# Kernel tuning notes

Hardware: AMD Instinct MI355X
Metric: run time of the kernel (lower is better)

The kernel has to match this reference:

```python
import jax, jax.numpy as jnp
import numpy as np

B = 32768
NMU = 3
K = 8
TMAX = 31.41592653589793
DE = 128
NC = 64
ZC = 1
IN_DIM = K + K * NMU  # 32

FREQS = jnp.asarray(1.0 / (np.float32(TMAX) ** np.arange(K // 2, dtype=np.float32)))


def _sinenc(x):
    # x: (B,) or (B,d) -> (B, K) or (B, d*K); per-feature [sin|cos] blocks concatenated
    if x.ndim == 1:
        xw = x[:, None] * FREQS[None, :]
        return jnp.concatenate([jnp.sin(xw), jnp.cos(xw)], axis=1)
    xw = x[:, :, None] * FREQS[None, None, :]  # (B, d, K/2)
    return jnp.concatenate([jnp.sin(xw), jnp.cos(xw)], axis=2).reshape(x.shape[0], -1)


def _conv3(x, w, b):
    y = jax.lax.conv_general_dilated(x, w, window_strides=(1, 1), padding=((1, 1), (1, 1)),
                                     dimension_numbers=("NCHW", "OIHW", "NCHW"))
    return y + b[None, :, None, None]


def setup_inputs() -> dict:
    key = jax.random.key(0)
    ks = jax.random.split(key, 20)
    s = 0.05
    return {
        "t": jax.random.uniform(ks[0], (B,), jnp.float32) * TMAX,
        "z": jax.random.normal(ks[1], (B, ZC, 4, 4), jnp.float32),
        "mu": jax.random.normal(ks[2], (B, NMU), jnp.float32),
        "W1": jax.random.normal(ks[3], (IN_DIM, DE), jnp.float32) * s,
        "b1": jnp.zeros((DE,), jnp.float32),
        "W2": jax.random.normal(ks[4], (DE, DE), jnp.float32) * s,
        "b2": jnp.zeros((DE,), jnp.float32),
        "Wg": jax.random.normal(ks[5], (DE, 4 * NC), jnp.float32) * s,
        "bg": jnp.zeros((4 * NC,), jnp.float32),
        "cin_w": jax.random.normal(ks[6], (NC, ZC, 3, 3), jnp.float32) * s,
        "cin_b": jnp.zeros((NC,), jnp.float32),
        "c1_w": jax.random.normal(ks[7], (NC, NC, 3, 3), jnp.float32) * s,
        "c1_b": jnp.zeros((NC,), jnp.float32),
        "c2_w": jax.random.normal(ks[8], (NC, NC, 3, 3), jnp.float32) * s,
        "c2_b": jnp.zeros((NC,), jnp.float32),
        "cout_w": jax.random.normal(ks[9], (ZC, NC, 3, 3), jnp.float32) * s,
        "cout_b": jnp.zeros((ZC,), jnp.float32),
    }


def reference(t, z, mu, W1, b1, W2, b2, Wg, bg,
              cin_w, cin_b, c1_w, c1_b, c2_w, c2_b, cout_w, cout_b):
    t_emb = _sinenc(t)            # (B, K)
    mu_emb = _sinenc(mu)          # (B, K*nmu)
    x = jnp.concatenate([t_emb, mu_emb], axis=1)  # (B, in_dim)
    h = jax.nn.elu(x @ W1 + b1)
    xi = jax.nn.elu(h @ W2 + b2)
    gb = (xi @ Wg + bg).reshape(-1, 4, NC)
    g1 = gb[:, 0][:, :, None, None]
    g2 = gb[:, 1][:, :, None, None]
    bb1 = gb[:, 2][:, :, None, None]
    bb2 = gb[:, 3][:, :, None, None]
    hh = jnp.tanh(_conv3(z, cin_w, cin_b))
    hh = jnp.tanh(g1 * _conv3(hh, c1_w, c1_b) + bb1)
    hh = jnp.tanh(g2 * _conv3(hh, c2_w, c2_b) + bb2)
    return _conv3(hh, cout_w, cout_b)
```

## Files before the change

kernel.cpp:

```cpp
#include <hip/hip_runtime.h>
#include <cstdint>
#include <cstddef>


#define NB 32768

typedef _Float16 half8   __attribute__((ext_vector_type(8)));
typedef _Float16 half4_t __attribute__((ext_vector_type(4)));
typedef _Float16 half2_t __attribute__((ext_vector_type(2)));
typedef float    f32x4   __attribute__((ext_vector_type(4)));

__device__ __forceinline__ float fast_tanh(float x) {
  float e = __expf(2.0f * x);
  return 1.0f - __fdividef(2.0f, e + 1.0f);
}

__device__ __forceinline__ float elu_f(float v) {
  return v > 0.0f ? v : (__expf(v) - 1.0f);
}

__device__ __forceinline__ void conv_acc(float acc[16], const float r[16], const float w[9]) {
#pragma unroll
  for (int y = 0; y < 4; ++y)
#pragma unroll
    for (int x = 0; x < 4; ++x)
#pragma unroll
      for (int ky = 0; ky < 3; ++ky) {
        int iy = y + ky - 1;
        if (iy < 0 || iy >= 4) continue;
#pragma unroll
        for (int kx = 0; kx < 3; ++kx) {
          int ix = x + kx - 1;
          if (ix < 0 || ix >= 4) continue;
          acc[y * 4 + x] += w[ky * 3 + kx] * r[iy * 4 + ix];
        }
      }
}

__global__ __launch_bounds__(256) void prep_kernel(
    const float* __restrict__ W1, const float* __restrict__ W2,
    const float* __restrict__ Wg, const float* __restrict__ c1w,
    const float* __restrict__ c2w, _Float16* __restrict__ wt) {
  int idx = blockIdx.x * 256 + threadIdx.x;
  _Float16* W1t = wt;
  _Float16* W2t = W1t + 4096;
  _Float16* Wgt = W2t + 16384;
  _Float16* c1t = Wgt + 32768;
  _Float16* c2t = c1t + 36864;
  if (idx < 4096) {
    int n = idx >> 5, k = idx & 31;
    W1t[idx] = (_Float16)W1[k * 128 + n];
  } else if (idx < 20480) {
    int i = idx - 4096;
    int n = i >> 7, k = i & 127;
    W2t[i] = (_Float16)W2[k * 128 + n];
  } else if (idx < 53248) {
    int i = idx - 20480;
    int n = i >> 7, k = i & 127;
    Wgt[i] = (_Float16)Wg[k * 256 + n];
  } else if (idx < 90112) {
    int i = idx - 53248;
    int ts = i >> 11, r = i & 2047, oc = r >> 5, icw = r & 31;
    int tap = ts >> 1, kb = ts & 1, ic = kb * 32 + icw;
    c1t[i] = (_Float16)c1w[(oc * 64 + ic) * 9 + tap];
  } else if (idx < 126976) {
    int i = idx - 90112;
    int ts = i >> 11, r = i & 2047, oc = r >> 5, icw = r & 31;
    int tap = ts >> 1, kb = ts & 1, ic = kb * 32 + icw;
    c2t[i] = (_Float16)c2w[(oc * 64 + ic) * 9 + tap];
  }
}

__global__ __launch_bounds__(256) void mlp_kernel(
    const float* __restrict__ tt, const float* __restrict__ mu,
    const _Float16* __restrict__ wt,
    const float* __restrict__ b1, const float* __restrict__ b2,
    const float* __restrict__ bg, _Float16* __restrict__ gbf) {
  const int tid = threadIdx.x;
  const int lane = tid & 63;
  const int wv = tid >> 6;
  const int m = lane & 15, q = lane >> 4;
  const int q4 = q * 4, q8 = q * 8;
  const int s = blockIdx.x * 64 + wv * 16 + m;

  const _Float16* W1t = wt;
  const _Float16* W2t = W1t + 4096;
  const _Float16* Wgt = W2t + 16384;

  __shared__ __align__(16) _Float16 xi_lds[4][16 * 136];
  _Float16* xw = &xi_lds[wv][0];

  const float TM = 31.41592653589793f;
  float base = (q == 0) ? tt[s] : mu[(size_t)s * 3 + (q - 1)];
  half8 xb;
  float fr = 1.0f;
#pragma unroll
  for (int j = 0; j < 4; ++j) {
    float sn, cs;
    __sincosf(base * fr, &sn, &cs);
    xb[j] = (_Float16)sn;
    xb[4 + j] = (_Float16)cs;
    fr *= (1.0f / TM);
  }

#pragma unroll
  for (int nt = 0; nt < 8; ++nt) {
    half8 af = *(const half8*)(W1t + (nt * 16 + m) * 32 + q8);
    f32x4 c = __builtin_amdgcn_mfma_f32_16x16x32_f16(af, xb, (f32x4)(0.0f), 0, 0, 0);
    f32x4 bv = *(const f32x4*)(b1 + nt * 16 + q4);
    half4_t o;
#pragma unroll
    for (int r = 0; r < 4; ++r) o[r] = (_Float16)elu_f(c[r] + bv[r]);
    *(half4_t*)(xw + m * 136 + nt * 16 + q4) = o;
  }
  half8 xf0 = *(const half8*)(xw + m * 136 + 0 + q8);
  half8 xf1 = *(const half8*)(xw + m * 136 + 32 + q8);
  half8 xf2 = *(const half8*)(xw + m * 136 + 64 + q8);
  half8 xf3 = *(const half8*)(xw + m * 136 + 96 + q8);

#pragma unroll
  for (int nt = 0; nt < 8; ++nt) {
    const _Float16* wp = W2t + (nt * 16 + m) * 128;
    f32x4 c = (f32x4)(0.0f);
    c = __builtin_amdgcn_mfma_f32_16x16x32_f16(*(const half8*)(wp + q8), xf0, c, 0, 0, 0);
    c = __builtin_amdgcn_mfma_f32_16x16x32_f16(*(const half8*)(wp + 32 + q8), xf1, c, 0, 0, 0);
    c = __builtin_amdgcn_mfma_f32_16x16x32_f16(*(const half8*)(wp + 64 + q8), xf2, c, 0, 0, 0);
    c = __builtin_amdgcn_mfma_f32_16x16x32_f16(*(const half8*)(wp + 96 + q8), xf3, c, 0, 0, 0);
    f32x4 bv = *(const f32x4*)(b2 + nt * 16 + q4);
    half4_t o;
#pragma unroll
    for (int r = 0; r < 4; ++r) o[r] = (_Float16)elu_f(c[r] + bv[r]);
    *(half4_t*)(xw + m * 136 + nt * 16 + q4) = o;
  }
  half8 yf0 = *(const half8*)(xw + m * 136 + 0 + q8);
  half8 yf1 = *(const half8*)(xw + m * 136 + 32 + q8);
  half8 yf2 = *(const half8*)(xw + m * 136 + 64 + q8);
  half8 yf3 = *(const half8*)(xw + m * 136 + 96 + q8);

#pragma unroll
  for (int ut = 0; ut < 16; ++ut) {
    const _Float16* wp = Wgt + (ut * 16 + m) * 128;
    f32x4 c = (f32x4)(0.0f);
    c = __builtin_amdgcn_mfma_f32_16x16x32_f16(*(const half8*)(wp + q8), yf0, c, 0, 0, 0);
    c = __builtin_amdgcn_mfma_f32_16x16x32_f16(*(const half8*)(wp + 32 + q8), yf1, c, 0, 0, 0);
    c = __builtin_amdgcn_mfma_f32_16x16x32_f16(*(const half8*)(wp + 64 + q8), yf2, c, 0, 0, 0);
    c = __builtin_amdgcn_mfma_f32_16x16x32_f16(*(const half8*)(wp + 96 + q8), yf3, c, 0, 0, 0);
    f32x4 bv = *(const f32x4*)(bg + ut * 16 + q4);
    half4_t o;
#pragma unroll
    for (int r = 0; r < 4; ++r) o[r] = (_Float16)(c[r] + bv[r]);
    *(half4_t*)(gbf + (size_t)s * 256 + ut * 16 + q4) = o;
  }
}

#define ROWE 72
#define SAMP 2592
#define GS 4
#define GRPS 16

__device__ __forceinline__ void mid_layer_mfma(
    const _Float16* __restrict__ src, _Float16* __restrict__ dst,
    const half8 af[18], const f32x4 cbv,
    const _Float16* __restrict__ gbase, int goff,
    int wv, int q, int py, int px) {
  f32x4 acc[GS];
#pragma unroll
  for (int g = 0; g < GS; ++g) acc[g] = (f32x4)(0.0f);
#pragma unroll
  for (int tap = 0; tap < 9; ++tap) {
    const int ky = tap / 3, kx = tap % 3;
    const int row = py + ky;
    const int pos = row * 6 + px + kx;
    const int e = (row ^ (pos >> 2)) & 1;
    const int o0 = pos * ROWE + q * 8 + e * 32;
    const int o1 = pos * ROWE + q * 8 + 32 - e * 32;
#pragma unroll
    for (int g = 0; g < GS; ++g) {
      half8 bb = *(const half8*)(src + g * SAMP + o0);
      acc[g] = __builtin_amdgcn_mfma_f32_16x16x32_f16(af[tap * 2 + 0], bb, acc[g], 0, 0, 0);
    }
#pragma unroll
    for (int g = 0; g < GS; ++g) {
      half8 bb = *(const half8*)(src + g * SAMP + o1);
      acc[g] = __builtin_amdgcn_mfma_f32_16x16x32_f16(af[tap * 2 + 1], bb, acc[g], 0, 0, 0);
    }
  }
  const int icb = wv * 16 + q * 4;
  const int row = 1 + py;
  const int pos = row * 6 + 1 + px;
  const int e = (row ^ (pos >> 2)) & 1;
  const int daddr = pos * ROWE + (((icb >> 5) ^ e) << 5) + (icb & 31);
#pragma unroll
  for (int g = 0; g < GS; ++g) {
    const _Float16* gp = gbase + g * 256 + goff + icb;
    half4_t gv = *(const half4_t*)(gp);
    half4_t bv = *(const half4_t*)(gp + 128);
    half4_t o;
#pragma unroll
    for (int r = 0; r < 4; ++r)
      o[r] = (_Float16)fast_tanh((float)gv[r] * (acc[g][r] + cbv[r]) + (float)bv[r]);
    *(half4_t*)(dst + g * SAMP + daddr) = o;
  }
}

__global__ __launch_bounds__(256, 2) void conv_kernel(
    const float* __restrict__ z, const _Float16* __restrict__ gbf,
    const float* __restrict__ cin_w, const float* __restrict__ cin_b,
    const _Float16* __restrict__ c1t, const _Float16* __restrict__ c2t,
    const float* __restrict__ c1_b, const float* __restrict__ c2_b,
    const float* __restrict__ cout_w, const float* __restrict__ cout_b,
    float* __restrict__ out) {
  const int tid = threadIdx.x;
  const int lane = tid & 63;
  const int wv = tid >> 6;
  const int s0 = blockIdx.x * (GRPS * GS);

  __shared__ __align__(16) _Float16 hp[2 * GS * SAMP];
  __shared__ __align__(16) _Float16 cwl[9 * 64];

  for (int i = tid; i < (2 * GS * SAMP) / 2; i += 256) ((uint32_t*)hp)[i] = 0u;
  for (int i = tid; i < 576; i += 256) {
    int ic = i / 9, tap = i % 9;
    cwl[tap * 64 + ic] = (_Float16)cout_w[i];
  }

  const int m = lane & 15, q = lane >> 4, q8 = q * 8, q4 = q * 4;
  const int py = m >> 2, px = m & 3;

  half8 a1f[18], a2f[18];
#pragma unroll
  for (int t = 0; t < 18; ++t) {
    a1f[t] = *(const half8*)(c1t + t * 2048 + (wv * 16 + m) * 32 + q8);
    a2f[t] = *(const half8*)(c2t + t * 2048 + (wv * 16 + m) * 32 + q8);
  }

  float cw9[9];
#pragma unroll
  for (int t = 0; t < 9; ++t) cw9[t] = cin_w[lane * 9 + t];
  const float cinb = cin_b[lane];
  const float cob = cout_b[0];
  const f32x4 cb1 = *(const f32x4*)(c1_b + wv * 16 + q4);
  const f32x4 cb2 = *(const f32x4*)(c2_b + wv * 16 + q4);

  __syncthreads();

  for (int grp = 0; grp < GRPS; ++grp) {
    const int sg = s0 + grp * GS;
    const _Float16* gbase = gbf + (size_t)sg * 256;

    {
      const float* zp = z + (size_t)(sg + wv) * 16;
      float r[16], acc[16];
#pragma unroll
      for (int p = 0; p < 16; ++p) { r[p] = zp[p]; acc[p] = 0.0f; }
      conv_acc(acc, r, cw9);
      _Float16* dst = hp + wv * SAMP;
      const int ics = lane & 31, ich = lane >> 5;
#pragma unroll
      for (int p = 0; p < 16; ++p) {
        int row = 1 + (p >> 2);
        int pos = row * 6 + 1 + (p & 3);
        int e = (row ^ (pos >> 2)) & 1;
        dst[pos * ROWE + ((ich ^ e) << 5) + ics] = (_Float16)fast_tanh(acc[p] + cinb);
      }
    }
    __syncthreads();

    mid_layer_mfma(hp, hp + GS * SAMP, a1f, cb1, gbase, 0, wv, q, py, px);
    __syncthreads();

    mid_layer_mfma(hp + GS * SAMP, hp, a2f, cb2, gbase, 64, wv, q, py, px);
    __syncthreads();

    {
      const _Float16* src = hp + wv * SAMP;
      const int c32 = q >> 1;
      const int coff = (q * 16) & 31;
      float acc = 0.0f;
#pragma unroll
      for (int tap = 0; tap < 9; ++tap) {
        const int ky = tap / 3, kx = tap % 3;
        const int row = py + ky;
        const int pos = row * 6 + px + kx;
        const int e = (row ^ (pos >> 2)) & 1;
        const _Float16* sp = src + pos * ROWE + ((c32 ^ e) << 5) + coff;
        half8 hv0 = *(const half8*)(sp);
        half8 hv1 = *(const half8*)(sp + 8);
        half8 wv0 = *(const half8*)(cwl + tap * 64 + q * 16);
        half8 wv1 = *(const half8*)(cwl + tap * 64 + q * 16 + 8);
#pragma unroll
        for (int j = 0; j < 4; ++j) {
          half2_t h2a = {hv0[2 * j], hv0[2 * j + 1]};
          half2_t w2a = {wv0[2 * j], wv0[2 * j + 1]};
          half2_t h2b = {hv1[2 * j], hv1[2 * j + 1]};
          half2_t w2b = {wv1[2 * j], wv1[2 * j + 1]};
#if __has_builtin(__builtin_amdgcn_fdot2)
          acc = __builtin_amdgcn_fdot2(h2a, w2a, acc, false);
          acc = __builtin_amdgcn_fdot2(h2b, w2b, acc, false);
#else
          acc += (float)h2a[0] * (float)w2a[0] + (float)h2a[1] * (float)w2a[1];
          acc += (float)h2b[0] * (float)w2b[0] + (float)h2b[1] * (float)w2b[1];
#endif
        }
      }
      acc += __shfl_xor(acc, 16);
      acc += __shfl_xor(acc, 32);
      if (q == 0) out[(size_t)(sg + wv) * 16 + m] = acc + cob;
    }
    __syncthreads();
  }
}

extern "C" void kernel_launch(void* const* d_in, const int* in_sizes, int n_in,
                              void* d_out, int out_size, void* d_ws, size_t ws_size,
                              hipStream_t stream) {
  const float* tt     = (const float*)d_in[0];
  const float* z      = (const float*)d_in[1];
  const float* mu     = (const float*)d_in[2];
  const float* W1     = (const float*)d_in[3];
  const float* b1     = (const float*)d_in[4];
  const float* W2     = (const float*)d_in[5];
  const float* b2     = (const float*)d_in[6];
  const float* Wg     = (const float*)d_in[7];
  const float* bg     = (const float*)d_in[8];
  const float* cin_w  = (const float*)d_in[9];
  const float* cin_b  = (const float*)d_in[10];
  const float* c1_w   = (const float*)d_in[11];
  const float* c1_b   = (const float*)d_in[12];
  const float* c2_w   = (const float*)d_in[13];
  const float* c2_b   = (const float*)d_in[14];
  const float* cout_w = (const float*)d_in[15];
  const float* cout_b = (const float*)d_in[16];

  float* out = (float*)d_out;
  _Float16* gbf = (_Float16*)d_ws;
  _Float16* wt  = gbf + (size_t)NB * 256;
  _Float16* W1t = wt;
  _Float16* W2t = W1t + 4096;
  _Float16* Wgt = W2t + 16384;
  _Float16* c1t = Wgt + 32768;
  _Float16* c2t = c1t + 36864;

  prep_kernel<<<496, 256, 0, stream>>>(W1, W2, Wg, c1_w, c2_w, wt);
  mlp_kernel<<<NB / 64, 256, 0, stream>>>(tt, mu, wt, b1, b2, bg, gbf);
  conv_kernel<<<NB / (GRPS * GS), 256, 0, stream>>>(z, gbf, cin_w, cin_b,
                                                    c1t, c2t, c1_b, c2_b,
                                                    cout_w, cout_b, out);
}
```

Measured before the change: 260.7 us.

## Fuse MLP into conv kernel, keeping gamma/beta in LDS with fragment-ordered weights

Removes the separate MLP kernel. Each conv block now computes the FiLM gamma/beta for its own 64 samples and stores them in shared memory (padded rows), instead of writing and re-reading a 16 MB fp16 buffer in global memory. The MLP weights are pre-permuted into MFMA fragment order so each lane does one contiguous 16-byte load. The extra LDS (about 33 KB) and register pressure may reduce occupancy of the conv kernel, and the MLP phase now runs serially inside each block.

```diff
diff --git a/kernel.cpp b/kernel.cpp
--- a/kernel.cpp
+++ b/kernel.cpp
@@ -42,22 +42,25 @@
     const float* __restrict__ Wg, const float* __restrict__ c1w,
     const float* __restrict__ c2w, _Float16* __restrict__ wt) {
   int idx = blockIdx.x * 256 + threadIdx.x;
-  _Float16* W1t = wt;
-  _Float16* W2t = W1t + 4096;
-  _Float16* Wgt = W2t + 16384;
-  _Float16* c1t = Wgt + 32768;
+  _Float16* W1f = wt;
+  _Float16* W2f = W1f + 4096;
+  _Float16* Wgf = W2f + 16384;
+  _Float16* c1t = Wgf + 32768;
   _Float16* c2t = c1t + 36864;
   if (idx < 4096) {
-    int n = idx >> 5, k = idx & 31;
-    W1t[idx] = (_Float16)W1[k * 128 + n];
+    int i = idx, j = i & 7, lane = (i >> 3) & 63, nt = i >> 9;
+    int n = nt * 16 + (lane & 15), k = (lane >> 4) * 8 + j;
+    W1f[i] = (_Float16)W1[k * 128 + n];
   } else if (idx < 20480) {
-    int i = idx - 4096;
-    int n = i >> 7, k = i & 127;
-    W2t[i] = (_Float16)W2[k * 128 + n];
+    int i = idx - 4096, j = i & 7, lane = (i >> 3) & 63, r = i >> 9;
+    int kb = r & 3, nt = r >> 2;
+    int n = nt * 16 + (lane & 15), k = kb * 32 + (lane >> 4) * 8 + j;
+    W2f[i] = (_Float16)W2[k * 128 + n];
   } else if (idx < 53248) {
-    int i = idx - 20480;
-    int n = i >> 7, k = i & 127;
-    Wgt[i] = (_Float16)Wg[k * 256 + n];
+    int i = idx - 20480, j = i & 7, lane = (i >> 3) & 63, r = i >> 9;
+    int kb = r & 3, ut = r >> 2;
+    int n = ut * 16 + (lane & 15), k = kb * 32 + (lane >> 4) * 8 + j;
+    Wgf[i] = (_Float16)Wg[k * 256 + n];
   } else if (idx < 90112) {
     int i = idx - 53248;
     int ts = i >> 11, r = i & 2047, oc = r >> 5, icw = r & 31;
@@ -71,92 +74,11 @@
   }
 }
 
-__global__ __launch_bounds__(256) void mlp_kernel(
-    const float* __restrict__ tt, const float* __restrict__ mu,
-    const _Float16* __restrict__ wt,
-    const float* __restrict__ b1, const float* __restrict__ b2,
-    const float* __restrict__ bg, _Float16* __restrict__ gbf) {
-  const int tid = threadIdx.x;
-  const int lane = tid & 63;
-  const int wv = tid >> 6;
-  const int m = lane & 15, q = lane >> 4;
-  const int q4 = q * 4, q8 = q * 8;
-  const int s = blockIdx.x * 64 + wv * 16 + m;
-
-  const _Float16* W1t = wt;
-  const _Float16* W2t = W1t + 4096;
-  const _Float16* Wgt = W2t + 16384;
-
-  __shared__ __align__(16) _Float16 xi_lds[4][16 * 136];
-  _Float16* xw = &xi_lds[wv][0];
-
-  const float TM = 31.41592653589793f;
-  float base = (q == 0) ? tt[s] : mu[(size_t)s * 3 + (q - 1)];
-  half8 xb;
-  float fr = 1.0f;
-#pragma unroll
-  for (int j = 0; j < 4; ++j) {
-    float sn, cs;
-    __sincosf(base * fr, &sn, &cs);
-    xb[j] = (_Float16)sn;
-    xb[4 + j] = (_Float16)cs;
-    fr *= (1.0f / TM);
-  }
-
-#pragma unroll
-  for (int nt = 0; nt < 8; ++nt) {
-    half8 af = *(const half8*)(W1t + (nt * 16 + m) * 32 + q8);
-    f32x4 c = __builtin_amdgcn_mfma_f32_16x16x32_f16(af, xb, (f32x4)(0.0f), 0, 0, 0);
-    f32x4 bv = *(const f32x4*)(b1 + nt * 16 + q4);
-    half4_t o;
-#pragma unroll
-    for (int r = 0; r < 4; ++r) o[r] = (_Float16)elu_f(c[r] + bv[r]);
-    *(half4_t*)(xw + m * 136 + nt * 16 + q4) = o;
-  }
-  half8 xf0 = *(const half8*)(xw + m * 136 + 0 + q8);
-  half8 xf1 = *(const half8*)(xw + m * 136 + 32 + q8);
-  half8 xf2 = *(const half8*)(xw + m * 136 + 64 + q8);
-  half8 xf3 = *(const half8*)(xw + m * 136 + 96 + q8);
-
-#pragma unroll
-  for (int nt = 0; nt < 8; ++nt) {
-    const _Float16* wp = W2t + (nt * 16 + m) * 128;
-    f32x4 c = (f32x4)(0.0f);
-    c = __builtin_amdgcn_mfma_f32_16x16x32_f16(*(const half8*)(wp + q8), xf0, c, 0, 0, 0);
-    c = __builtin_amdgcn_mfma_f32_16x16x32_f16(*(const half8*)(wp + 32 + q8), xf1, c, 0, 0, 0);
-    c = __builtin_amdgcn_mfma_f32_16x16x32_f16(*(const half8*)(wp + 64 + q8), xf2, c, 0, 0, 0);
-    c = __builtin_amdgcn_mfma_f32_16x16x32_f16(*(const half8*)(wp + 96 + q8), xf3, c, 0, 0, 0);
-    f32x4 bv = *(const f32x4*)(b2 + nt * 16 + q4);
-    half4_t o;
-#pragma unroll
-    for (int r = 0; r < 4; ++r) o[r] = (_Float16)elu_f(c[r] + bv[r]);
-    *(half4_t*)(xw + m * 136 + nt * 16 + q4) = o;
-  }
-  half8 yf0 = *(const half8*)(xw + m * 136 + 0 + q8);
-  half8 yf1 = *(const half8*)(xw + m * 136 + 32 + q8);
-  half8 yf2 = *(const half8*)(xw + m * 136 + 64 + q8);
-  half8 yf3 = *(const half8*)(xw + m * 136 + 96 + q8);
-
-#pragma unroll
-  for (int ut = 0; ut < 16; ++ut) {
-    const _Float16* wp = Wgt + (ut * 16 + m) * 128;
-    f32x4 c = (f32x4)(0.0f);
-    c = __builtin_amdgcn_mfma_f32_16x16x32_f16(*(const half8*)(wp + q8), yf0, c, 0, 0, 0);
-    c = __builtin_amdgcn_mfma_f32_16x16x32_f16(*(const half8*)(wp + 32 + q8), yf1, c, 0, 0, 0);
-    c = __builtin_amdgcn_mfma_f32_16x16x32_f16(*(const half8*)(wp + 64 + q8), yf2, c, 0, 0, 0);
-    c = __builtin_amdgcn_mfma_f32_16x16x32_f16(*(const half8*)(wp + 96 + q8), yf3, c, 0, 0, 0);
-    f32x4 bv = *(const f32x4*)(bg + ut * 16 + q4);
-    half4_t o;
-#pragma unroll
-    for (int r = 0; r < 4; ++r) o[r] = (_Float16)(c[r] + bv[r]);
-    *(half4_t*)(gbf + (size_t)s * 256 + ut * 16 + q4) = o;
-  }
-}
-
 #define ROWE 72
 #define SAMP 2592
 #define GS 4
 #define GRPS 16
+#define GBROW 264
 
 __device__ __forceinline__ void mid_layer_mfma(
     const _Float16* __restrict__ src, _Float16* __restrict__ dst,
@@ -192,7 +114,7 @@
   const int daddr = pos * ROWE + (((icb >> 5) ^ e) << 5) + (icb & 31);
 #pragma unroll
   for (int g = 0; g < GS; ++g) {
-    const _Float16* gp = gbase + g * 256 + goff + icb;
+    const _Float16* gp = gbase + g * GBROW + goff + icb;
     half4_t gv = *(const half4_t*)(gp);
     half4_t bv = *(const half4_t*)(gp + 128);
     half4_t o;
@@ -203,29 +125,99 @@
   }
 }
 
-__global__ __launch_bounds__(256, 2) void conv_kernel(
-    const float* __restrict__ z, const _Float16* __restrict__ gbf,
+__global__ __launch_bounds__(256, 2) void fused_kernel(
+    const float* __restrict__ tt, const float* __restrict__ mu,
+    const float* __restrict__ z, const _Float16* __restrict__ wt,
+    const float* __restrict__ b1, const float* __restrict__ b2,
+    const float* __restrict__ bg,
     const float* __restrict__ cin_w, const float* __restrict__ cin_b,
-    const _Float16* __restrict__ c1t, const _Float16* __restrict__ c2t,
     const float* __restrict__ c1_b, const float* __restrict__ c2_b,
     const float* __restrict__ cout_w, const float* __restrict__ cout_b,
     float* __restrict__ out) {
   const int tid = threadIdx.x;
   const int lane = tid & 63;
   const int wv = tid >> 6;
-  const int s0 = blockIdx.x * (GRPS * GS);
-
-  __shared__ __align__(16) _Float16 hp[2 * GS * SAMP];
-  __shared__ __align__(16) _Float16 cwl[9 * 64];
-
-  for (int i = tid; i < (2 * GS * SAMP) / 2; i += 256) ((uint32_t*)hp)[i] = 0u;
-  for (int i = tid; i < 576; i += 256) {
-    int ic = i / 9, tap = i % 9;
-    cwl[tap * 64 + ic] = (_Float16)cout_w[i];
-  }
-
   const int m = lane & 15, q = lane >> 4, q8 = q * 8, q4 = q * 4;
   const int py = m >> 2, px = m & 3;
+  const int s0 = blockIdx.x * (GRPS * GS);
+
+  const _Float16* W1f = wt;
+  const _Float16* W2f = W1f + 4096;
+  const _Float16* Wgf = W2f + 16384;
+  const _Float16* c1t = Wgf + 32768;
+  const _Float16* c2t = c1t + 36864;
+
+  __shared__ __align__(16) _Float16 hp[2 * GS * SAMP];
+  __shared__ __align__(16) _Float16 gb_lds[64 * GBROW];
+  __shared__ __align__(16) _Float16 cwl[9 * 64];
+
+  {
+    const int sl = wv * 16 + m;
+    const int s = s0 + sl;
+    _Float16* xw = hp + wv * SAMP;
+
+    const float TM = 31.41592653589793f;
+    float base = (q == 0) ? tt[s] : mu[(size_t)s * 3 + (q - 1)];
+    half8 xb;
+    float fr = 1.0f;
+#pragma unroll
+    for (int j = 0; j < 4; ++j) {
+      float sn, cs;
+      __sincosf(base * fr, &sn, &cs);
+      xb[j] = (_Float16)sn;
+      xb[4 + j] = (_Float16)cs;
+      fr *= (1.0f / TM);
+    }
+
+#pragma unroll
+    for (int nt = 0; nt < 8; ++nt) {
+      half8 af = *(const half8*)(W1f + (nt * 64 + lane) * 8);
+      f32x4 c = __builtin_amdgcn_mfma_f32_16x16x32_f16(af, xb, (f32x4)(0.0f), 0, 0, 0);
+      f32x4 bv = *(const f32x4*)(b1 + nt * 16 + q4);
+      half4_t o;
+#pragma unroll
+      for (int r = 0; r < 4; ++r) o[r] = (_Float16)elu_f(c[r] + bv[r]);
+      *(half4_t*)(xw + m * 136 + nt * 16 + q4) = o;
+    }
+    half8 xf0 = *(const half8*)(xw + m * 136 + 0 + q8);
+    half8 xf1 = *(const half8*)(xw + m * 136 + 32 + q8);
+    half8 xf2 = *(const half8*)(xw + m * 136 + 64 + q8);
+    half8 xf3 = *(const half8*)(xw + m * 136 + 96 + q8);
+
+#pragma unroll
+    for (int nt = 0; nt < 8; ++nt) {
+      const _Float16* wp = W2f + (nt * 4) * 512 + lane * 8;
+      f32x4 c = (f32x4)(0.0f);
+      c = __builtin_amdgcn_mfma_f32_16x16x32_f16(*(const half8*)(wp), xf0, c, 0, 0, 0);
+      c = __builtin_amdgcn_mfma_f32_16x16x32_f16(*(const half8*)(wp + 512), xf1, c, 0, 0, 0);
+      c = __builtin_amdgcn_mfma_f32_16x16x32_f16(*(const half8*)(wp + 1024), xf2, c, 0, 0, 0);
+      c = __builtin_amdgcn_mfma_f32_16x16x32_f16(*(const half8*)(wp + 1536), xf3, c, 0, 0, 0);
+      f32x4 bv = *(const f32x4*)(b2 + nt * 16 + q4);
+      half4_t o;
+#pragma unroll
+      for (int r = 0; r < 4; ++r) o[r] = (_Float16)elu_f(c[r] + bv[r]);
+      *(half4_t*)(xw + m * 136 + nt * 16 + q4) = o;
+    }
+    half8 yf0 = *(const half8*)(xw + m * 136 + 0 + q8);
+    half8 yf1 = *(const half8*)(xw + m * 136 + 32 + q8);
+    half8 yf2 = *(const half8*)(xw + m * 136 + 64 + q8);
+    half8 yf3 = *(const half8*)(xw + m * 136 + 96 + q8);
+
+#pragma unroll
+    for (int ut = 0; ut < 16; ++ut) {
+      const _Float16* wp = Wgf + (ut * 4) * 512 + lane * 8;
+      f32x4 c = (f32x4)(0.0f);
+      c = __builtin_amdgcn_mfma_f32_16x16x32_f16(*(const half8*)(wp), yf0, c, 0, 0, 0);
+      c = __builtin_amdgcn_mfma_f32_16x16x32_f16(*(const half8*)(wp + 512), yf1, c, 0, 0, 0);
+      c = __builtin_amdgcn_mfma_f32_16x16x32_f16(*(const half8*)(wp + 1024), yf2, c, 0, 0, 0);
+      c = __builtin_amdgcn_mfma_f32_16x16x32_f16(*(const half8*)(wp + 1536), yf3, c, 0, 0, 0);
+      f32x4 bv = *(const f32x4*)(bg + ut * 16 + q4);
+      half4_t o;
+#pragma unroll
+      for (int r = 0; r < 4; ++r) o[r] = (_Float16)(c[r] + bv[r]);
+      *(half4_t*)(gb_lds + sl * GBROW + ut * 16 + q4) = o;
+    }
+  }
 
   half8 a1f[18], a2f[18];
 #pragma unroll
@@ -233,7 +225,6 @@
     a1f[t] = *(const half8*)(c1t + t * 2048 + (wv * 16 + m) * 32 + q8);
     a2f[t] = *(const half8*)(c2t + t * 2048 + (wv * 16 + m) * 32 + q8);
   }
-
   float cw9[9];
 #pragma unroll
   for (int t = 0; t < 9; ++t) cw9[t] = cin_w[lane * 9 + t];
@@ -244,9 +235,16 @@
 
   __syncthreads();
 
+  for (int i = tid; i < (2 * GS * SAMP) / 2; i += 256) ((uint32_t*)hp)[i] = 0u;
+  for (int i = tid; i < 576; i += 256) {
+    int ic = i / 9, tap = i % 9;
+    cwl[tap * 64 + ic] = (_Float16)cout_w[i];
+  }
+  __syncthreads();
+
   for (int grp = 0; grp < GRPS; ++grp) {
     const int sg = s0 + grp * GS;
-    const _Float16* gbase = gbf + (size_t)sg * 256;
+    const _Float16* gbase = gb_lds + (size_t)(grp * GS) * GBROW;
 
     {
       const float* zp = z + (size_t)(sg + wv) * 16;
@@ -333,17 +331,9 @@
   const float* cout_b = (const float*)d_in[16];
 
   float* out = (float*)d_out;
-  _Float16* gbf = (_Float16*)d_ws;
-  _Float16* wt  = gbf + (size_t)NB * 256;
-  _Float16* W1t = wt;
-  _Float16* W2t = W1t + 4096;
-  _Float16* Wgt = W2t + 16384;
-  _Float16* c1t = Wgt + 32768;
-  _Float16* c2t = c1t + 36864;
+  _Float16* wt = (_Float16*)d_ws;
 
   prep_kernel<<<496, 256, 0, stream>>>(W1, W2, Wg, c1_w, c2_w, wt);
-  mlp_kernel<<<NB / 64, 256, 0, stream>>>(tt, mu, wt, b1, b2, bg, gbf);
-  conv_kernel<<<NB / (GRPS * GS), 256, 0, stream>>>(z, gbf, cin_w, cin_b,
-                                                    c1t, c2t, c1_b, c2_b,
-                                                    cout_w, cout_b, out);
-}
+  fused_kernel<<<NB / (GRPS * GS), 256, 0, stream>>>(
+      tt, mu, z, wt, b1, b2, bg, cin_w, cin_b, c1_b, c2_b, cout_w, cout_b, out);
+}
```

Measured after the change: 226.6 us. 13.1% less time.
